# Performance work log

Measured on AMD Instinct MI355X. Metric: run time of the kernel, lower is better.

The kernel has to match this reference:

```python
import jax, jax.numpy as jnp
import numpy as np

D_MODEL = 1024
N_HEADS = 16
D_HEAD = D_MODEL // N_HEADS
RANK = 16
DECAY = 0.95
ALPHA_MAX = 0.05
BETA = 0.01


def setup_inputs() -> dict:
    key = jax.random.key(0)
    ks = jax.random.split(key, 9)
    B, T = 4, 2048
    s = 0.02  # init scale for weights
    return {
        "hidden_states": jax.random.normal(ks[0], (B, T, D_MODEL), jnp.float32),
        "m_gate": jax.random.uniform(ks[1], (B, T), jnp.float32),
        "alpha_scale": jax.random.uniform(ks[2], (B, T, N_HEADS), jnp.float32),
        "Wq": jax.random.normal(ks[3], (D_MODEL, D_MODEL), jnp.float32) * s,
        "Wk": jax.random.normal(ks[4], (D_MODEL, D_MODEL), jnp.float32) * s,
        "Wv": jax.random.normal(ks[5], (D_MODEL, D_MODEL), jnp.float32) * s,
        "Wo": jax.random.normal(ks[6], (D_MODEL, D_MODEL), jnp.float32) * s,
        "Wa": jax.random.normal(ks[7], (N_HEADS, D_MODEL), jnp.float32) * s,
        "ba": jnp.zeros((N_HEADS,), jnp.float32),
        "mix_logit": jnp.zeros((N_HEADS,), jnp.float32),
    }


def reference(hidden_states, m_gate, alpha_scale, Wq, Wk, Wv, Wo, Wa, ba, mix_logit):
    B, T, D = hidden_states.shape
    H, Dh, R = N_HEADS, D_HEAD, RANK
    # batched projections (Linear: x @ W.T), then split heads
    q = (hidden_states @ Wq.T).reshape(B, T, H, Dh)
    k = (hidden_states @ Wk.T).reshape(B, T, H, Dh)
    v = (hidden_states @ Wv.T).reshape(B, T, H, Dh)
    # alpha computed under torch.no_grad in the original -> stop_gradient
    alpha = jax.nn.sigmoid(hidden_states @ Wa.T + ba)  # [B,T,H]
    alpha = alpha * m_gate[..., None] * alpha_scale
    alpha = jnp.minimum(alpha, ALPHA_MAX)
    alpha = jax.lax.stop_gradient(alpha)

    inv_sqrt_dh = 1.0 / (Dh ** 0.5)

    def step(carry, xs):
        U, V = carry  # U: [B,H,Dh,R], V: [B,H,R,Dh]
        q_t, k_t, v_t, a_t = xs  # [B,H,Dh], [B,H,Dh], [B,H,Dh], [B,H]
        U = DECAY * U
        V = DECAY * V
        ku = jnp.einsum('bhd,bhdr->bhr', k_t, U)
        a = a_t[..., None, None]
        U = U + a * jnp.einsum('bhd,bhr->bhdr', k_t, ku)
        V = V + a * jnp.einsum('bhr,bhd->bhrd', ku, v_t)
        U = U - BETA * jnp.clip(U, -1.0, 1.0)
        V = V - BETA * jnp.clip(V, -1.0, 1.0)
        # whole fast-weight update is no_grad in the original
        U = jax.lax.stop_gradient(U)
        V = jax.lax.stop_gradient(V)
        q_norm = q_t * inv_sqrt_dh
        k_fast = jnp.einsum('bhdr,bhrd->bhd', U, V)  # [B,H,Dh]
        score_slow = jnp.sum(q_norm * k_t, axis=-1)  # [B,H]
        score_fast = jnp.sum(q_norm * k_fast, axis=-1)
        logits = jnp.stack([score_slow, score_fast], axis=-1) + mix_logit[None, :, None]
        mix = jax.nn.softmax(logits, axis=-1)  # [B,H,2]
        y = mix[..., 0:1] * v_t + mix[..., 1:2] * k_fast  # [B,H,Dh]
        return (U, V), y

    U0 = jnp.zeros((B, H, Dh, R), hidden_states.dtype)
    V0 = jnp.zeros((B, H, R, Dh), hidden_states.dtype)
    xs = (jnp.moveaxis(q, 1, 0), jnp.moveaxis(k, 1, 0),
          jnp.moveaxis(v, 1, 0), jnp.moveaxis(alpha, 1, 0))
    _, ys = jax.lax.scan(step, (U0, V0), xs)  # ys: [T,B,H,Dh]
    y = jnp.moveaxis(ys, 0, 1).reshape(B, T, D)
    return y @ Wo.T
```

## Files before the change

### kernel.cpp

```cpp
#include <hip/hip_runtime.h>
#include <hip/hip_bf16.h>
#include <stdint.h>

#define D_MODEL 1024
#define N_HEADS 16
#define D_HEAD  64
#define SEQ_T   2048
#define BATCH   4

typedef unsigned short u16;
typedef __bf16 bf16x8 __attribute__((ext_vector_type(8)));
typedef float  f32x4  __attribute__((ext_vector_type(4)));

#define NT 32
#define BUF 4096

__device__ __forceinline__ u16 f2bf(float x) {
  unsigned u = __float_as_uint(x);
  u += 0x7fffu + ((u >> 16) & 1u);
  return (u16)(u >> 16);
}
__device__ __forceinline__ unsigned pk2(float a, float b) {
  return (unsigned)f2bf(a) | ((unsigned)f2bf(b) << 16);
}
__device__ __forceinline__ unsigned scale2(unsigned p, float s) {
  float lo = __uint_as_float(p << 16) * s;
  float hi = __uint_as_float(p & 0xffff0000u) * s;
  return pk2(lo, hi);
}

__global__ __launch_bounds__(256) void cast_kernel(const float* __restrict__ hs,
                                                   const float* __restrict__ wq,
                                                   const float* __restrict__ wk,
                                                   const float* __restrict__ wv,
                                                   const float* __restrict__ wo,
                                                   u16* __restrict__ Xb,
                                                   u16* __restrict__ Wb) {
  int i = blockIdx.x * 256 + threadIdx.x;
  const float* src; u16* dst; int soff, doff;
  if (i < (2 << 20)) {
    src = hs; dst = Xb; soff = i; doff = i;
  } else {
    int j = i - (2 << 20);
    int R = j >> 8;
    int col4 = j & 255;
    int srow;
    if (R < 2048) {
      int h = R >> 7, c = R & 127, jj = c >> 4, l = c & 15;
      srow = h * 64 + (jj >> 1) * 16 + l;
      src = (jj & 1) ? wk : wq;
    } else if (R < 3072) { src = wv; srow = R - 2048; }
    else                 { src = wo; srow = R - 3072; }
    dst = Wb; soff = srow * 256 + col4; doff = R * 256 + col4;
  }
  float4 v = ((const float4*)src)[soff];
  uint2 o; o.x = pk2(v.x, v.y); o.y = pk2(v.z, v.w);
  ((uint2*)dst)[doff] = o;
}

__global__ __launch_bounds__(256, 4) void gemm_qkv_kernel(const u16* __restrict__ A,
                                                          const u16* __restrict__ B,
                                                          u16* __restrict__ Vb,
                                                          float* __restrict__ S) {
  constexpr int K = D_MODEL;
  __shared__ u16 As[2 * BUF];
  __shared__ u16 Bs[2 * BUF];
  const int tid  = threadIdx.x;
  const int lane = tid & 63;
  const int wave = tid >> 6;
  const int wm = (wave >> 1) * 64;
  const int wn = (wave & 1) * 64;
  const int bm = blockIdx.y * 128;
  const int bn = blockIdx.x;
  const int quad = lane >> 4;
  const int l16  = lane & 15;
  const int rchunk = quad ^ ((l16 >> 1) & 3);

  const int lr = tid >> 2;
  const int lch = tid & 3;
  const int wch = lch ^ ((lr >> 1) & 3);
  const u16* Ap0 = A + (size_t)(bm + lr) * K + lch * 8;
  const u16* Ap1 = Ap0 + (size_t)64 * K;
  const u16* Bp0 = B + (size_t)(bn * 128 + lr) * K + lch * 8;
  const u16* Bp1 = Bp0 + (size_t)64 * K;
  u16* Aw0 = As + lr * 32 + wch * 8;
  u16* Aw1 = Aw0 + 64 * 32;
  u16* Bw0 = Bs + lr * 32 + wch * 8;
  u16* Bw1 = Bw0 + 64 * 32;

  f32x4 acc[4][4];
  #pragma unroll
  for (int i = 0; i < 4; ++i)
    #pragma unroll
    for (int j = 0; j < 4; ++j) acc[i][j] = (f32x4){0.f, 0.f, 0.f, 0.f};

  uint4 a0 = *(const uint4*)Ap0;
  uint4 a1 = *(const uint4*)Ap1;
  uint4 b0 = *(const uint4*)Bp0;
  uint4 b1 = *(const uint4*)Bp1;
  *(uint4*)Aw0 = a0; *(uint4*)Aw1 = a1;
  *(uint4*)Bw0 = b0; *(uint4*)Bw1 = b1;
  a0 = *(const uint4*)(Ap0 + 32);
  a1 = *(const uint4*)(Ap1 + 32);
  b0 = *(const uint4*)(Bp0 + 32);
  b1 = *(const uint4*)(Bp1 + 32);
  __syncthreads();

  #pragma unroll 2
  for (int t = 0; t < NT; ++t) {
    const int p = t & 1;
    const u16* Ar = As + p * BUF;
    const u16* Br = Bs + p * BUF;
    bf16x8 af[4], bfr[4];
    #pragma unroll
    for (int i = 0; i < 4; ++i)
      af[i] = *(const bf16x8*)(Ar + (wm + i * 16 + l16) * 32 + rchunk * 8);
    #pragma unroll
    for (int j = 0; j < 4; ++j)
      bfr[j] = *(const bf16x8*)(Br + (wn + j * 16 + l16) * 32 + rchunk * 8);
    if (t + 1 < NT) {
      const int q = (p ^ 1) * BUF;
      *(uint4*)(Aw0 + q) = a0; *(uint4*)(Aw1 + q) = a1;
      *(uint4*)(Bw0 + q) = b0; *(uint4*)(Bw1 + q) = b1;
      if (t + 2 < NT) {
        const int o = (t + 2) * 32;
        a0 = *(const uint4*)(Ap0 + o);
        a1 = *(const uint4*)(Ap1 + o);
        b0 = *(const uint4*)(Bp0 + o);
        b1 = *(const uint4*)(Bp1 + o);
      }
    }
    #pragma unroll
    for (int i = 0; i < 4; ++i)
      #pragma unroll
      for (int j = 0; j < 4; ++j)
        acc[i][j] = __builtin_amdgcn_mfma_f32_16x16x32_bf16(af[i], bfr[j], acc[i][j], 0, 0, 0);
    __syncthreads();
  }

  if (bn < N_HEADS) {
    float part[4][4];
    #pragma unroll
    for (int i = 0; i < 4; ++i)
      #pragma unroll
      for (int e = 0; e < 4; ++e)
        part[i][e] = acc[i][0][e] * acc[i][1][e] + acc[i][2][e] * acc[i][3][e];
    #pragma unroll
    for (int m = 1; m <= 8; m <<= 1)
      #pragma unroll
      for (int i = 0; i < 4; ++i)
        #pragma unroll
        for (int e = 0; e < 4; ++e)
          part[i][e] += __shfl_xor(part[i][e], m);
    __syncthreads();
    float* Sp = (float*)As;
    if (l16 == 0) {
      #pragma unroll
      for (int i = 0; i < 4; ++i)
        #pragma unroll
        for (int e = 0; e < 4; ++e)
          Sp[(wm + i * 16 + quad * 4 + e) * 2 + (wave & 1)] = part[i][e];
    }
    __syncthreads();
    if (tid < 128) {
      float s = (Sp[tid * 2] + Sp[tid * 2 + 1]) * 0.125f;
      S[(size_t)(bm + tid) * N_HEADS + bn] = 1.f / (1.f + __expf(-s));
    }
  } else {
    const int cb = (bn - N_HEADS) * 128;
    #pragma unroll
    for (int i = 0; i < 4; ++i)
      #pragma unroll
      for (int j = 0; j < 4; ++j)
        #pragma unroll
        for (int e = 0; e < 4; ++e) {
          int row = bm + wm + i * 16 + quad * 4 + e;
          int col = cb + wn + j * 16 + l16;
          Vb[(size_t)row * D_MODEL + col] = f2bf(acc[i][j][e]);
        }
  }
}

__global__ __launch_bounds__(256, 4) void gemm_out_kernel(const u16* __restrict__ A,
                                                          const u16* __restrict__ B,
                                                          const float* __restrict__ S,
                                                          float* __restrict__ C) {
  constexpr int K = D_MODEL, N = D_MODEL;
  __shared__ u16 As[2 * BUF];
  __shared__ u16 Bs[2 * BUF];
  const int tid  = threadIdx.x;
  const int lane = tid & 63;
  const int wave = tid >> 6;
  const int wm = (wave >> 1) * 64;
  const int wn = (wave & 1) * 64;
  const int bm = blockIdx.y * 128;
  const int bn = blockIdx.x * 128;
  const int quad = lane >> 4;
  const int l16  = lane & 15;
  const int rchunk = quad ^ ((l16 >> 1) & 3);

  const int lr = tid >> 2;
  const int lch = tid & 3;
  const int wch = lch ^ ((lr >> 1) & 3);
  const u16* Ap0 = A + (size_t)(bm + lr) * K + lch * 8;
  const u16* Ap1 = Ap0 + (size_t)64 * K;
  const u16* Bp0 = B + (size_t)(bn + lr) * K + lch * 8;
  const u16* Bp1 = Bp0 + (size_t)64 * K;
  u16* Aw0 = As + lr * 32 + wch * 8;
  u16* Aw1 = Aw0 + 64 * 32;
  u16* Bw0 = Bs + lr * 32 + wch * 8;
  u16* Bw1 = Bw0 + 64 * 32;
  const float* Sp0 = S + (size_t)(bm + lr) * N_HEADS;
  const float* Sp1 = Sp0 + (size_t)64 * N_HEADS;

  f32x4 acc[4][4];
  #pragma unroll
  for (int i = 0; i < 4; ++i)
    #pragma unroll
    for (int j = 0; j < 4; ++j) acc[i][j] = (f32x4){0.f, 0.f, 0.f, 0.f};

  uint4 a0 = *(const uint4*)Ap0;
  uint4 a1 = *(const uint4*)Ap1;
  uint4 b0 = *(const uint4*)Bp0;
  uint4 b1 = *(const uint4*)Bp1;
  float rs0 = Sp0[0], rs1 = Sp1[0];
  {
    uint4 w0, w1;
    w0.x = scale2(a0.x, rs0); w0.y = scale2(a0.y, rs0);
    w0.z = scale2(a0.z, rs0); w0.w = scale2(a0.w, rs0);
    w1.x = scale2(a1.x, rs1); w1.y = scale2(a1.y, rs1);
    w1.z = scale2(a1.z, rs1); w1.w = scale2(a1.w, rs1);
    *(uint4*)Aw0 = w0; *(uint4*)Aw1 = w1;
    *(uint4*)Bw0 = b0; *(uint4*)Bw1 = b1;
  }
  a0 = *(const uint4*)(Ap0 + 32);
  a1 = *(const uint4*)(Ap1 + 32);
  b0 = *(const uint4*)(Bp0 + 32);
  b1 = *(const uint4*)(Bp1 + 32);
  __syncthreads();

  #pragma unroll 2
  for (int t = 0; t < NT; ++t) {
    const int p = t & 1;
    const u16* Ar = As + p * BUF;
    const u16* Br = Bs + p * BUF;
    bf16x8 af[4], bfr[4];
    #pragma unroll
    for (int i = 0; i < 4; ++i)
      af[i] = *(const bf16x8*)(Ar + (wm + i * 16 + l16) * 32 + rchunk * 8);
    #pragma unroll
    for (int j = 0; j < 4; ++j)
      bfr[j] = *(const bf16x8*)(Br + (wn + j * 16 + l16) * 32 + rchunk * 8);
    if (t + 1 < NT) {
      const int q = (p ^ 1) * BUF;
      uint4 w0, w1;
      w0.x = scale2(a0.x, rs0); w0.y = scale2(a0.y, rs0);
      w0.z = scale2(a0.z, rs0); w0.w = scale2(a0.w, rs0);
      w1.x = scale2(a1.x, rs1); w1.y = scale2(a1.y, rs1);
      w1.z = scale2(a1.z, rs1); w1.w = scale2(a1.w, rs1);
      *(uint4*)(Aw0 + q) = w0; *(uint4*)(Aw1 + q) = w1;
      *(uint4*)(Bw0 + q) = b0; *(uint4*)(Bw1 + q) = b1;
      if (t + 2 < NT) {
        const int o = (t + 2) * 32;
        a0 = *(const uint4*)(Ap0 + o);
        a1 = *(const uint4*)(Ap1 + o);
        b0 = *(const uint4*)(Bp0 + o);
        b1 = *(const uint4*)(Bp1 + o);
        rs0 = Sp0[(t + 2) >> 1];
        rs1 = Sp1[(t + 2) >> 1];
      }
    }
    #pragma unroll
    for (int i = 0; i < 4; ++i)
      #pragma unroll
      for (int j = 0; j < 4; ++j)
        acc[i][j] = __builtin_amdgcn_mfma_f32_16x16x32_bf16(af[i], bfr[j], acc[i][j], 0, 0, 0);
    __syncthreads();
  }

  #pragma unroll
  for (int i = 0; i < 4; ++i)
    #pragma unroll
    for (int j = 0; j < 4; ++j)
      #pragma unroll
      for (int e = 0; e < 4; ++e) {
        int row = bm + wm + i * 16 + quad * 4 + e;
        int col = bn + wn + j * 16 + l16;
        C[(size_t)row * N + col] = acc[i][j][e];
      }
}

extern "C" void kernel_launch(void* const* d_in, const int* in_sizes, int n_in,
                              void* d_out, int out_size, void* d_ws, size_t ws_size,
                              hipStream_t stream) {
  const float* hs = (const float*)d_in[0];
  const float* Wq = (const float*)d_in[3];
  const float* Wk = (const float*)d_in[4];
  const float* Wv = (const float*)d_in[5];
  const float* Wo = (const float*)d_in[6];

  char* ws = (char*)d_ws;
  u16*  Xb = (u16*)ws;
  u16*  Wb = (u16*)(ws + (16u << 20));
  u16*  Vb = (u16*)(ws + (24u << 20));
  float* Sb = (float*)(ws + (40u << 20));
  float* out = (float*)d_out;

  cast_kernel<<<12288, 256, 0, stream>>>(hs, Wq, Wk, Wv, Wo, Xb, Wb);
  gemm_qkv_kernel<<<dim3(24, 64), 256, 0, stream>>>(Xb, Wb, Vb, Sb);
  gemm_out_kernel<<<dim3(8, 64), 256, 0, stream>>>(
      Vb, Wb + (size_t)3072 * D_MODEL, Sb, out);
}
```

Before: 214.4 us.

## Load out-projection B tiles via direct global-to-LDS and widen cast kernel

In the output GEMM, the B (Wo) tile is now fetched with global_load_lds, which writes straight into shared memory and skips the staging registers and explicit LDS stores. The address swizzle moves from the write side to the global read side so it matches the existing XOR read pattern. The cast kernel now converts 8 floats per thread with 16-byte stores instead of 4, which halves the grid. Risks: the direct-to-LDS copies have no explicit wait before the barrier, and the LDS layout must match what the MFMA fragment reads expect.

Result: faster. 204.9 us (-4.5%).

```diff
diff --git a/kernel.cpp b/kernel.cpp
--- a/kernel.cpp
+++ b/kernel.cpp
@@ -27,6 +27,11 @@
   float lo = __uint_as_float(p << 16) * s;
   float hi = __uint_as_float(p & 0xffff0000u) * s;
   return pk2(lo, hi);
+}
+__device__ __forceinline__ void cp16(const u16* g, u16* l) {
+  __builtin_amdgcn_global_load_lds(
+      (const __attribute__((address_space(1))) unsigned int*)g,
+      (__attribute__((address_space(3))) unsigned int*)l, 16, 0, 0);
 }
 
 __global__ __launch_bounds__(256) void cast_kernel(const float* __restrict__ hs,
@@ -36,26 +41,31 @@
                                                    const float* __restrict__ wo,
                                                    u16* __restrict__ Xb,
                                                    u16* __restrict__ Wb) {
-  int i = blockIdx.x * 256 + threadIdx.x;
-  const float* src; u16* dst; int soff, doff;
-  if (i < (2 << 20)) {
-    src = hs; dst = Xb; soff = i; doff = i;
+  int g = blockIdx.x * 256 + threadIdx.x;
+  const float4* src; uint4* dst;
+  if (g < (1 << 20)) {
+    src = (const float4*)hs + 2 * (size_t)g;
+    dst = (uint4*)Xb + g;
   } else {
-    int j = i - (2 << 20);
-    int R = j >> 8;
-    int col4 = j & 255;
+    int j = g - (1 << 20);
+    int R = j >> 7;
+    int col8 = j & 127;
+    const float* s;
     int srow;
     if (R < 2048) {
       int h = R >> 7, c = R & 127, jj = c >> 4, l = c & 15;
       srow = h * 64 + (jj >> 1) * 16 + l;
-      src = (jj & 1) ? wk : wq;
-    } else if (R < 3072) { src = wv; srow = R - 2048; }
-    else                 { src = wo; srow = R - 3072; }
-    dst = Wb; soff = srow * 256 + col4; doff = R * 256 + col4;
-  }
-  float4 v = ((const float4*)src)[soff];
-  uint2 o; o.x = pk2(v.x, v.y); o.y = pk2(v.z, v.w);
-  ((uint2*)dst)[doff] = o;
+      s = (jj & 1) ? wk : wq;
+    } else if (R < 3072) { s = wv; srow = R - 2048; }
+    else                 { s = wo; srow = R - 3072; }
+    src = (const float4*)s + (size_t)srow * 256 + col8 * 2;
+    dst = (uint4*)Wb + (size_t)R * 128 + col8;
+  }
+  float4 lo = src[0], hi = src[1];
+  uint4 o;
+  o.x = pk2(lo.x, lo.y); o.y = pk2(lo.z, lo.w);
+  o.z = pk2(hi.x, hi.y); o.w = pk2(hi.z, hi.w);
+  *dst = o;
 }
 
 __global__ __launch_bounds__(256, 4) void gemm_qkv_kernel(const u16* __restrict__ A,
@@ -204,14 +214,16 @@
   const int wch = lch ^ ((lr >> 1) & 3);
   const u16* Ap0 = A + (size_t)(bm + lr) * K + lch * 8;
   const u16* Ap1 = Ap0 + (size_t)64 * K;
-  const u16* Bp0 = B + (size_t)(bn + lr) * K + lch * 8;
-  const u16* Bp1 = Bp0 + (size_t)64 * K;
   u16* Aw0 = As + lr * 32 + wch * 8;
   u16* Aw1 = Aw0 + 64 * 32;
-  u16* Bw0 = Bs + lr * 32 + wch * 8;
-  u16* Bw1 = Bw0 + 64 * 32;
   const float* Sp0 = S + (size_t)(bm + lr) * N_HEADS;
   const float* Sp1 = Sp0 + (size_t)64 * N_HEADS;
+
+  const int srow = lane >> 2;
+  const int gch  = (lane & 3) ^ ((lane >> 3) & 3);
+  const u16* Bg0 = B + (size_t)(bn + wave * 16 + srow) * K + gch * 8;
+  const u16* Bg1 = Bg0 + (size_t)64 * K;
+  u16* Bl = Bs + wave * 16 * 32 + lane * 8;
 
   f32x4 acc[4][4];
   #pragma unroll
@@ -221,9 +233,8 @@
 
   uint4 a0 = *(const uint4*)Ap0;
   uint4 a1 = *(const uint4*)Ap1;
-  uint4 b0 = *(const uint4*)Bp0;
-  uint4 b1 = *(const uint4*)Bp1;
   float rs0 = Sp0[0], rs1 = Sp1[0];
+  cp16(Bg0, Bl);           cp16(Bg1, Bl + 64 * 32);
   {
     uint4 w0, w1;
     w0.x = scale2(a0.x, rs0); w0.y = scale2(a0.y, rs0);
@@ -231,12 +242,9 @@
     w1.x = scale2(a1.x, rs1); w1.y = scale2(a1.y, rs1);
     w1.z = scale2(a1.z, rs1); w1.w = scale2(a1.w, rs1);
     *(uint4*)Aw0 = w0; *(uint4*)Aw1 = w1;
-    *(uint4*)Bw0 = b0; *(uint4*)Bw1 = b1;
   }
   a0 = *(const uint4*)(Ap0 + 32);
   a1 = *(const uint4*)(Ap1 + 32);
-  b0 = *(const uint4*)(Bp0 + 32);
-  b1 = *(const uint4*)(Bp1 + 32);
   __syncthreads();
 
   #pragma unroll 2
@@ -253,19 +261,18 @@
       bfr[j] = *(const bf16x8*)(Br + (wn + j * 16 + l16) * 32 + rchunk * 8);
     if (t + 1 < NT) {
       const int q = (p ^ 1) * BUF;
+      cp16(Bg0 + (t + 1) * 32, Bl + q);
+      cp16(Bg1 + (t + 1) * 32, Bl + q + 64 * 32);
       uint4 w0, w1;
       w0.x = scale2(a0.x, rs0); w0.y = scale2(a0.y, rs0);
       w0.z = scale2(a0.z, rs0); w0.w = scale2(a0.w, rs0);
       w1.x = scale2(a1.x, rs1); w1.y = scale2(a1.y, rs1);
       w1.z = scale2(a1.z, rs1); w1.w = scale2(a1.w, rs1);
       *(uint4*)(Aw0 + q) = w0; *(uint4*)(Aw1 + q) = w1;
-      *(uint4*)(Bw0 + q) = b0; *(uint4*)(Bw1 + q) = b1;
       if (t + 2 < NT) {
         const int o = (t + 2) * 32;
         a0 = *(const uint4*)(Ap0 + o);
         a1 = *(const uint4*)(Ap1 + o);
-        b0 = *(const uint4*)(Bp0 + o);
-        b1 = *(const uint4*)(Bp1 + o);
         rs0 = Sp0[(t + 2) >> 1];
         rs1 = Sp1[(t + 2) >> 1];
       }
@@ -306,7 +313,7 @@
   float* Sb = (float*)(ws + (40u << 20));
   float* out = (float*)d_out;
 
-  cast_kernel<<<12288, 256, 0, stream>>>(hs, Wq, Wk, Wv, Wo, Xb, Wb);
+  cast_kernel<<<6144, 256, 0, stream>>>(hs, Wq, Wk, Wv, Wo, Xb, Wb);
   gemm_qkv_kernel<<<dim3(24, 64), 256, 0, stream>>>(Xb, Wb, Vb, Sb);
   gemm_out_kernel<<<dim3(8, 64), 256, 0, stream>>>(
       Vb, Wb + (size_t)3072 * D_MODEL, Sb, out);
```
